# Kernel tuning notes

Hardware: AMD Instinct MI355X
Metric: run time of the kernel (lower is better)

The kernel has to match this reference:

```python
import jax, jax.numpy as jnp
import numpy as np

N, T, H, D, E, P, R = 50000, 16, 512, 256, 200000, 100000, 3
LN_EPS = 1e-5
BN_EPS = 1e-5


def setup_inputs() -> dict:
    key = jax.random.key(0)
    ks = jax.random.split(key, 32)
    ri = lambda k, shape, hi: jax.random.randint(k, shape, 0, hi)
    rn = lambda k, shape, scale=0.05: (jax.random.normal(k, shape, dtype=jnp.float32) * scale)
    return {
        "node_type_ids": ri(ks[0], (N,), T),
        "src0": ri(ks[1], (E,), N), "dst0": ri(ks[2], (E,), N),
        "src1": ri(ks[3], (E,), N), "dst1": ri(ks[4], (E,), N),
        "src2": ri(ks[5], (E,), N), "dst2": ri(ks[6], (E,), N),
        "pairs": ri(ks[7], (2, P), N),
        "degrees": ri(ks[8], (N,), 100),
        "node_emb": rn(ks[9], (N, H)),
        "type_emb": rn(ks[10], (T, H)),
        "w_loop_in": rn(ks[11], (H, H)),
        "w_rel_in": rn(ks[12], (R, H, H)),
        "w_loop_res": rn(ks[13], (H, H)),
        "w_rel_res": rn(ks[14], (R, H, H)),
        "ln_g": jnp.ones((H,), jnp.float32),
        "ln_b": jnp.zeros((H,), jnp.float32),
        "w_loop_out": rn(ks[15], (H, D)),
        "w_rel_out": rn(ks[16], (R, H, D)),
        "lp_w1": rn(ks[17], (3 * D, D)),
        "lp_b1": jnp.zeros((D,), jnp.float32),
        "bn_g": jnp.ones((D,), jnp.float32),
        "bn_b": jnp.zeros((D,), jnp.float32),
        "bn_mean": jnp.zeros((D,), jnp.float32),
        "bn_var": jnp.ones((D,), jnp.float32),
        "lp_w2": rn(ks[18], (D, 1)),
        "lp_b2": jnp.zeros((1,), jnp.float32),
        "alpha": jnp.float32(0.1),
        "beta": jnp.float32(0.1),
    }


def _rgcn(x, loop_w, rel_w, srcs, dsts):
    # out = x @ W_loop + sum_r (A_r @ x) @ W_r ; A_r unweighted COO -> segment_sum
    out = x @ loop_w
    for r in range(R):
        msg = jax.ops.segment_sum(x[srcs[r]], dsts[r], num_segments=x.shape[0])
        out = out + msg @ rel_w[r]
    return out


def _layernorm(h, g, b):
    mu = h.mean(-1, keepdims=True)
    var = h.var(-1, keepdims=True)
    return (h - mu) * jax.lax.rsqrt(var + LN_EPS) * g + b


def reference(node_type_ids, src0, dst0, src1, dst1, src2, dst2, pairs, degrees,
              node_emb, type_emb, w_loop_in, w_rel_in, w_loop_res, w_rel_res,
              ln_g, ln_b, w_loop_out, w_rel_out, lp_w1, lp_b1, bn_g, bn_b,
              bn_mean, bn_var, lp_w2, lp_b2, alpha, beta):
    srcs = (src0, src1, src2)
    dsts = (dst0, dst1, dst2)
    # encode
    x = node_emb + type_emb[node_type_ids]          # [N, H]
    x = jax.nn.relu(_rgcn(x, w_loop_in, w_rel_in, srcs, dsts))
    h = _rgcn(x, w_loop_res, w_rel_res, srcs, dsts)
    h = jax.nn.relu(_layernorm(h, ln_g, ln_b))      # dropout p=0 -> identity
    x = x + h
    z = _rgcn(x, w_loop_out, w_rel_out, srcs, dsts)  # [N, D]
    # score
    src_z = z[pairs[0]]                              # [P, D]
    dst_z = z[pairs[1]]
    src_deg = jnp.clip(degrees[pairs[0]], 1).astype(jnp.float32)
    dst_deg = jnp.clip(degrees[pairs[1]], 1).astype(jnp.float32)
    feats = jnp.concatenate([src_z, dst_z, src_z * dst_z], axis=-1)  # [P, 3D]
    h1 = jax.nn.relu(feats @ lp_w1 + lp_b1)
    # BatchNorm1d in eval mode: running stats
    h1 = (h1 - bn_mean) * jax.lax.rsqrt(bn_var + BN_EPS) * bn_g + bn_b
    mlp_score = (h1 @ lp_w2 + lp_b2).squeeze(-1)     # [P]
    base = mlp_score - jax.nn.relu(alpha) * jnp.log(src_deg) - jax.nn.relu(beta) * jnp.log(dst_deg)
    return base / (jnp.sqrt(src_deg) * jnp.sqrt(dst_deg) + 1e-8)
```

## Files before the change

### kernel.cpp

```cpp
#include <hip/hip_runtime.h>

typedef __attribute__((ext_vector_type(8))) _Float16 half8;
typedef __attribute__((ext_vector_type(4))) _Float16 half4;
typedef __attribute__((ext_vector_type(4))) float f32x4;

static __device__ __forceinline__ void gload16(const void* g, void* l) {
  __builtin_amdgcn_global_load_lds((const __attribute__((address_space(1))) void*)g,
                                   (__attribute__((address_space(3))) void*)l, 16, 0, 0);
}

__global__ void k_encode(const float* __restrict__ emb, const float* __restrict__ temb,
                         const int* __restrict__ tids, _Float16* __restrict__ x, int n) {
  int i = blockIdx.x * 256 + threadIdx.x;
  if (i >= n * 64) return;
  int node = i >> 6, c = (i & 63) << 3;
  const float* e = emb + (size_t)node * 512 + c;
  const float* t = temb + (size_t)tids[node] * 512 + c;
  float4 a0 = *(const float4*)e, a1 = *(const float4*)(e + 4);
  float4 b0 = *(const float4*)t, b1 = *(const float4*)(t + 4);
  half8 o;
  o[0] = (_Float16)(a0.x + b0.x); o[1] = (_Float16)(a0.y + b0.y);
  o[2] = (_Float16)(a0.z + b0.z); o[3] = (_Float16)(a0.w + b0.w);
  o[4] = (_Float16)(a1.x + b1.x); o[5] = (_Float16)(a1.y + b1.y);
  o[6] = (_Float16)(a1.z + b1.z); o[7] = (_Float16)(a1.w + b1.w);
  *(half8*)(x + (size_t)node * 512 + c) = o;
}

__global__ void k_hist(const int* __restrict__ d0, const int* __restrict__ d1,
                       const int* __restrict__ d2, int* __restrict__ counts, int E) {
  int e = blockIdx.x * 256 + threadIdx.x;
  if (e >= E) return;
  int r = blockIdx.y;
  const int* d = (r == 0) ? d0 : ((r == 1) ? d1 : d2);
  atomicAdd(&counts[d[e] + 1], 1);
}

__global__ void k_scan(const int* __restrict__ counts, int* __restrict__ rowp,
                       int* __restrict__ cursor, int n) {
  __shared__ int wsum[16];
  int lane = threadIdx.x & 63, w = threadIdx.x >> 6;
  int off = 0;
  for (int base = 0; base < n; base += 1024) {
    int i = base + threadIdx.x;
    int v = (i < n) ? counts[i] : 0;
    int sc = v;
    #pragma unroll
    for (int d = 1; d < 64; d <<= 1) {
      int t = __shfl_up(sc, (unsigned)d);
      if (lane >= d) sc += t;
    }
    if (lane == 63) wsum[w] = sc;
    __syncthreads();
    int wo = 0, tot = 0;
    #pragma unroll
    for (int ww = 0; ww < 16; ++ww) {
      int s = wsum[ww];
      if (ww < w) wo += s;
      tot += s;
    }
    if (i < n) { int val = sc + wo + off; rowp[i] = val; cursor[i] = val; }
    off += tot;
    __syncthreads();
  }
}

__global__ void k_fill(const int* __restrict__ s0, const int* __restrict__ s1, const int* __restrict__ s2,
                       const int* __restrict__ d0, const int* __restrict__ d1, const int* __restrict__ d2,
                       int* __restrict__ cursor, int* __restrict__ colrel, int E) {
  int e = blockIdx.x * 256 + threadIdx.x;
  if (e >= E) return;
  int r = blockIdx.y;
  const int* dp = (r == 0) ? d0 : ((r == 1) ? d1 : d2);
  const int* sp = (r == 0) ? s0 : ((r == 1) ? s1 : s2);
  int pos = atomicAdd(&cursor[dp[e]], 1);
  if (pos >= 0 && pos < 3 * E) colrel[pos] = sp[e] | (r << 24);
}

__global__ void k_aggregate(const _Float16* __restrict__ x, _Float16* __restrict__ agg,
                            const int* __restrict__ rowp, const int* __restrict__ colrel,
                            int N) {
  int wid = (blockIdx.x * 256 + threadIdx.x) >> 6;
  int lane = threadIdx.x & 63;
  if (wid >= N) return;
  int beg = rowp[wid], end = rowp[wid + 1];
  int co = lane * 8;
  float a0[8] = {0,0,0,0,0,0,0,0}, a1[8] = {0,0,0,0,0,0,0,0}, a2[8] = {0,0,0,0,0,0,0,0};
  int e = beg;
  for (; e + 4 <= end; e += 4) {
    int c0 = colrel[e], c1 = colrel[e + 1], c2 = colrel[e + 2], c3 = colrel[e + 3];
    half8 v0 = *(const half8*)(x + (size_t)(c0 & 0xFFFFFF) * 512 + co);
    half8 v1 = *(const half8*)(x + (size_t)(c1 & 0xFFFFFF) * 512 + co);
    half8 v2 = *(const half8*)(x + (size_t)(c2 & 0xFFFFFF) * 512 + co);
    half8 v3 = *(const half8*)(x + (size_t)(c3 & 0xFFFFFF) * 512 + co);
    {
      int r = c0 >> 24;
      if (r == 0) { for (int j = 0; j < 8; ++j) a0[j] += (float)v0[j]; }
      else if (r == 1) { for (int j = 0; j < 8; ++j) a1[j] += (float)v0[j]; }
      else { for (int j = 0; j < 8; ++j) a2[j] += (float)v0[j]; }
    }
    {
      int r = c1 >> 24;
      if (r == 0) { for (int j = 0; j < 8; ++j) a0[j] += (float)v1[j]; }
      else if (r == 1) { for (int j = 0; j < 8; ++j) a1[j] += (float)v1[j]; }
      else { for (int j = 0; j < 8; ++j) a2[j] += (float)v1[j]; }
    }
    {
      int r = c2 >> 24;
      if (r == 0) { for (int j = 0; j < 8; ++j) a0[j] += (float)v2[j]; }
      else if (r == 1) { for (int j = 0; j < 8; ++j) a1[j] += (float)v2[j]; }
      else { for (int j = 0; j < 8; ++j) a2[j] += (float)v2[j]; }
    }
    {
      int r = c3 >> 24;
      if (r == 0) { for (int j = 0; j < 8; ++j) a0[j] += (float)v3[j]; }
      else if (r == 1) { for (int j = 0; j < 8; ++j) a1[j] += (float)v3[j]; }
      else { for (int j = 0; j < 8; ++j) a2[j] += (float)v3[j]; }
    }
  }
  for (; e < end; ++e) {
    int c0 = colrel[e];
    half8 v0 = *(const half8*)(x + (size_t)(c0 & 0xFFFFFF) * 512 + co);
    int r = c0 >> 24;
    if (r == 0) { for (int j = 0; j < 8; ++j) a0[j] += (float)v0[j]; }
    else if (r == 1) { for (int j = 0; j < 8; ++j) a1[j] += (float)v0[j]; }
    else { for (int j = 0; j < 8; ++j) a2[j] += (float)v0[j]; }
  }
  half8 o0, o1, o2;
  #pragma unroll
  for (int j = 0; j < 8; ++j) {
    o0[j] = (_Float16)a0[j]; o1[j] = (_Float16)a1[j]; o2[j] = (_Float16)a2[j];
  }
  size_t ob = (size_t)wid * 1536;
  *(half8*)(agg + ob + co) = o0;
  *(half8*)(agg + ob + 512 + co) = o1;
  *(half8*)(agg + ob + 1024 + co) = o2;
}

__global__ void k_transpose_all(const float* __restrict__ wli, const float* __restrict__ wri,
                                const float* __restrict__ wlr, const float* __restrict__ wrr,
                                const float* __restrict__ wlo, const float* __restrict__ wro,
                                const float* __restrict__ lpw1,
                                _Float16* __restrict__ Bti, _Float16* __restrict__ Btr,
                                _Float16* __restrict__ Bto, _Float16* __restrict__ Btl) {
  __shared__ float tile[64][65];
  int zi = blockIdx.z;
  const float* Bl; const float* Br; _Float16* Bt; int No, K;
  if (zi == 0)      { Bl = wli;  Br = wri;            Bt = Bti; No = 512; K = 2048; }
  else if (zi == 1) { Bl = wlr;  Br = wrr;            Bt = Btr; No = 512; K = 2048; }
  else if (zi == 2) { Bl = wlo;  Br = wro;            Bt = Bto; No = 256; K = 2048; }
  else              { Bl = lpw1; Br = lpw1 + 512*256; Bt = Btl; No = 256; K = 768;  }
  int k0 = blockIdx.x * 64, n0 = blockIdx.y * 64;
  if (k0 >= K || n0 >= No) return;
  int nl = threadIdx.x & 63, kb = threadIdx.x >> 6;
  #pragma unroll
  for (int i = 0; i < 16; ++i) {
    int kl = kb + i * 4;
    int krow = k0 + kl;
    float v = (krow < 512) ? Bl[(size_t)krow * No + n0 + nl]
                           : Br[(size_t)(krow - 512) * No + n0 + nl];
    tile[kl][nl] = v;
  }
  __syncthreads();
  int kl = threadIdx.x & 63, nb = threadIdx.x >> 6;
  #pragma unroll
  for (int i = 0; i < 16; ++i) {
    int n2 = nb + i * 4;
    Bt[(size_t)(n0 + n2) * K + k0 + kl] = (_Float16)tile[kl][n2];
  }
}

__global__ __launch_bounds__(512) void k_gemm_rgcn(
    const _Float16* __restrict__ Ain, const _Float16* __restrict__ Aagg,
    const _Float16* __restrict__ Bt, _Float16* __restrict__ C,
    int M, int Ncols, int K, int relu, int S, int T) {
  __shared__ __align__(16) _Float16 As[256 * 64];
  __shared__ __align__(16) _Float16 Bs[128 * 64];
  int lin = blockIdx.x;
  int grp = lin / (8 * T);
  int rmd = lin - grp * 8 * T;
  int c = rmd >> 3, x = rmd & 7;
  int s = grp * 8 + x;
  if (s >= S) return;
  int bm0 = s * 256, bn0 = c * 128;

  int tid = threadIdx.x;
  int lane = tid & 63, wv = tid >> 6;
  int wm = wv & 3, wn = wv >> 2;
  int l16 = lane & 15, quad = lane >> 4;

  int rl8 = lane >> 3;
  int gs = (lane & 7) ^ rl8;

  int rA[4];
  const _Float16* pa[4];
  const _Float16* pb[2];
  _Float16* ldA[4];
  _Float16* ldB[2];
  #pragma unroll
  for (int q = 0; q < 4; ++q) {
    int chunk = wv * 4 + q;
    int rl = chunk * 8 + rl8;
    int ra = bm0 + rl; if (ra >= M) ra = M - 1;
    rA[q] = ra;
    pa[q] = Ain + (size_t)ra * 512 + gs * 8;
    ldA[q] = &As[chunk * 8 * 64];
  }
  #pragma unroll
  for (int q = 0; q < 2; ++q) {
    int chunk = wv * 2 + q;
    int rl = chunk * 8 + rl8;
    pb[q] = Bt + (size_t)(bn0 + rl) * K + gs * 8;
    ldB[q] = &Bs[chunk * 8 * 64];
  }

  f32x4 acc[4][4];
  #pragma unroll
  for (int i = 0; i < 4; ++i)
    #pragma unroll
    for (int j = 0; j < 4; ++j) acc[i][j] = (f32x4){0.f, 0.f, 0.f, 0.f};

  for (int k0 = 0; k0 < K; k0 += 64) {
    if (k0 == 512) {
      #pragma unroll
      for (int q = 0; q < 4; ++q) pa[q] = Aagg + (size_t)rA[q] * 1536 + gs * 8;
    }
    __syncthreads();
    #pragma unroll
    for (int q = 0; q < 4; ++q) gload16(pa[q], ldA[q]);
    #pragma unroll
    for (int q = 0; q < 2; ++q) gload16(pb[q], ldB[q]);
    __syncthreads();
    #pragma unroll
    for (int sb = 0; sb < 2; ++sb) {
      half8 af[4], bf[4];
      int slot = ((sb * 4 + quad) ^ (l16 & 7)) * 8;
      #pragma unroll
      for (int i = 0; i < 4; ++i)
        af[i] = *(const half8*)&As[(wm * 64 + i * 16 + l16) * 64 + slot];
      #pragma unroll
      for (int j = 0; j < 4; ++j)
        bf[j] = *(const half8*)&Bs[(wn * 64 + j * 16 + l16) * 64 + slot];
      #pragma unroll
      for (int i = 0; i < 4; ++i)
        #pragma unroll
        for (int j = 0; j < 4; ++j)
          acc[i][j] = __builtin_amdgcn_mfma_f32_16x16x32_f16(af[i], bf[j], acc[i][j], 0, 0, 0);
    }
    #pragma unroll
    for (int q = 0; q < 4; ++q) pa[q] += 64;
    #pragma unroll
    for (int q = 0; q < 2; ++q) pb[q] += 64;
  }

  #pragma unroll
  for (int i = 0; i < 4; ++i)
    #pragma unroll
    for (int j = 0; j < 4; ++j)
      #pragma unroll
      for (int rg = 0; rg < 4; ++rg) {
        int row = bm0 + wm * 64 + i * 16 + quad * 4 + rg;
        int col = bn0 + wn * 64 + j * 16 + l16;
        if (row < M) {
          float v = acc[i][j][rg];
          if (relu) v = fmaxf(v, 0.f);
          C[(size_t)row * Ncols + col] = (_Float16)v;
        }
      }
}

#define LSTR 40

__global__ __launch_bounds__(256) void k_gemm_link(
    const _Float16* __restrict__ z, const int* __restrict__ pairs,
    const _Float16* __restrict__ Bt,
    const float* __restrict__ b1, const float* __restrict__ bng, const float* __restrict__ bnb,
    const float* __restrict__ bnm, const float* __restrict__ bnv,
    _Float16* __restrict__ h1, int P, int K) {
  __shared__ __align__(16) _Float16 As[128 * LSTR];
  __shared__ __align__(16) _Float16 Bs[128 * LSTR];
  int tid = threadIdx.x;
  int bn0 = blockIdx.x * 128, bm0 = blockIdx.y * 128;
  int lane = tid & 63, wv = tid >> 6;
  int wm = wv & 1, wn = wv >> 1;
  int l16 = lane & 15, quad = lane >> 4;
  int srow = tid >> 1, scs = (tid & 1) * 16;
  int p = bm0 + srow; if (p >= P) p = P - 1;
  int sp = pairs[p], dp = pairs[P + p];
  const _Float16* zs = z + (size_t)sp * 256;
  const _Float16* zd = z + (size_t)dp * 256;
  int bgn = bn0 + srow;

  f32x4 acc[4][4];
  #pragma unroll
  for (int i = 0; i < 4; ++i)
    #pragma unroll
    for (int j = 0; j < 4; ++j) acc[i][j] = (f32x4){0.f, 0.f, 0.f, 0.f};

  for (int k0 = 0; k0 < K; k0 += 32) {
    __syncthreads();
    int seg = k0 >> 8;
    int kk = (k0 & 255) + scs;
    __attribute__((aligned(16))) _Float16 tmp[16];
    if (seg == 0) {
      *(uint4*)tmp = *(const uint4*)(zs + kk);
      *(uint4*)(tmp + 8) = *(const uint4*)(zs + kk + 8);
    } else if (seg == 1) {
      *(uint4*)tmp = *(const uint4*)(zd + kk);
      *(uint4*)(tmp + 8) = *(const uint4*)(zd + kk + 8);
    } else {
      half8 u0 = *(const half8*)(zs + kk), u1 = *(const half8*)(zs + kk + 8);
      half8 v0 = *(const half8*)(zd + kk), v1 = *(const half8*)(zd + kk + 8);
      #pragma unroll
      for (int j = 0; j < 8; ++j) {
        tmp[j] = (_Float16)((float)u0[j] * (float)v0[j]);
        tmp[j + 8] = (_Float16)((float)u1[j] * (float)v1[j]);
      }
    }
    *(uint4*)&As[srow * LSTR + scs] = *(const uint4*)tmp;
    *(uint4*)&As[srow * LSTR + scs + 8] = *(const uint4*)(tmp + 8);
    {
      const _Float16* src = Bt + (size_t)bgn * K + k0 + scs;
      *(uint4*)&Bs[srow * LSTR + scs] = *(const uint4*)src;
      *(uint4*)&Bs[srow * LSTR + scs + 8] = *(const uint4*)(src + 8);
    }
    __syncthreads();
    half8 af[4], bf[4];
    #pragma unroll
    for (int i = 0; i < 4; ++i)
      af[i] = *(const half8*)&As[(wm * 64 + i * 16 + l16) * LSTR + quad * 8];
    #pragma unroll
    for (int j = 0; j < 4; ++j)
      bf[j] = *(const half8*)&Bs[(wn * 64 + j * 16 + l16) * LSTR + quad * 8];
    #pragma unroll
    for (int i = 0; i < 4; ++i)
      #pragma unroll
      for (int j = 0; j < 4; ++j)
        acc[i][j] = __builtin_amdgcn_mfma_f32_16x16x32_f16(af[i], bf[j], acc[i][j], 0, 0, 0);
  }

  #pragma unroll
  for (int i = 0; i < 4; ++i)
    #pragma unroll
    for (int j = 0; j < 4; ++j) {
      int col = bn0 + wn * 64 + j * 16 + l16;
      float bb1 = b1[col], m = bnm[col], rs = rsqrtf(bnv[col] + 1e-5f);
      float gg = bng[col], bb = bnb[col];
      #pragma unroll
      for (int rg = 0; rg < 4; ++rg) {
        int row = bm0 + wm * 64 + i * 16 + quad * 4 + rg;
        if (row < P) {
          float v = fmaxf(acc[i][j][rg] + bb1, 0.f);
          v = (v - m) * rs * gg + bb;
          h1[(size_t)row * 256 + col] = (_Float16)v;
        }
      }
    }
}

__global__ void k_ln_res(const _Float16* __restrict__ h, const _Float16* __restrict__ x1,
                         const float* __restrict__ g, const float* __restrict__ b,
                         _Float16* __restrict__ out, int N) {
  int wid = (blockIdx.x * 256 + threadIdx.x) >> 6;
  int lane = threadIdx.x & 63;
  if (wid >= N) return;
  int c = lane * 8;
  half8 hv = *(const half8*)(h + (size_t)wid * 512 + c);
  float hf[8];
  float s = 0.f, sq = 0.f;
  #pragma unroll
  for (int j = 0; j < 8; ++j) {
    hf[j] = (float)hv[j];
    s += hf[j];
    sq += hf[j] * hf[j];
  }
  #pragma unroll
  for (int off = 32; off; off >>= 1) {
    s += __shfl_down(s, (unsigned)off);
    sq += __shfl_down(sq, (unsigned)off);
  }
  s = __shfl(s, 0); sq = __shfl(sq, 0);
  float mu = s * (1.f / 512.f);
  float var = sq * (1.f / 512.f) - mu * mu;
  float rs = rsqrtf(var + 1e-5f);
  float4 g0 = *(const float4*)(g + c), g1 = *(const float4*)(g + c + 4);
  float4 b0 = *(const float4*)(b + c), b1 = *(const float4*)(b + c + 4);
  float gf[8] = {g0.x, g0.y, g0.z, g0.w, g1.x, g1.y, g1.z, g1.w};
  float bf[8] = {b0.x, b0.y, b0.z, b0.w, b1.x, b1.y, b1.z, b1.w};
  half8 xv = *(const half8*)(x1 + (size_t)wid * 512 + c);
  half8 o;
  #pragma unroll
  for (int j = 0; j < 8; ++j) {
    float xw = (float)xv[j];
    o[j] = (_Float16)(xw + fmaxf((hf[j] - mu) * rs * gf[j] + bf[j], 0.f));
  }
  *(half8*)(out + (size_t)wid * 512 + c) = o;
}

__global__ void k_score(const _Float16* __restrict__ h1, const float* __restrict__ w2,
                        const float* __restrict__ b2, const int* __restrict__ pairs,
                        const int* __restrict__ degrees, const float* __restrict__ alpha,
                        const float* __restrict__ beta, float* __restrict__ out, int P) {
  int wid = (blockIdx.x * 256 + threadIdx.x) >> 6;
  int lane = threadIdx.x & 63;
  if (wid >= P) return;
  int c = lane * 4;
  half4 hv = *(const half4*)(h1 + (size_t)wid * 256 + c);
  float4 wv = *(const float4*)(w2 + c);
  float s = (float)hv[0] * wv.x + (float)hv[1] * wv.y + (float)hv[2] * wv.z + (float)hv[3] * wv.w;
  #pragma unroll
  for (int off = 32; off; off >>= 1) s += __shfl_down(s, (unsigned)off);
  if (lane == 0) {
    int sp = pairs[wid], dp = pairs[P + wid];
    float sd = (float)max(degrees[sp], 1);
    float dd = (float)max(degrees[dp], 1);
    float base = s + b2[0] - fmaxf(alpha[0], 0.f) * logf(sd) - fmaxf(beta[0], 0.f) * logf(dd);
    out[wid] = base / (sqrtf(sd) * sqrtf(dd) + 1e-8f);
  }
}

extern "C" void kernel_launch(void* const* d_in, const int* in_sizes, int n_in,
                              void* d_out, int out_size, void* d_ws, size_t ws_size,
                              hipStream_t stream) {
  const int N = 50000, E = 200000, P = 100000;
  const int Np1 = N + 1;
  const int* node_type = (const int*)d_in[0];
  const int* src0 = (const int*)d_in[1]; const int* dst0 = (const int*)d_in[2];
  const int* src1 = (const int*)d_in[3]; const int* dst1 = (const int*)d_in[4];
  const int* src2 = (const int*)d_in[5]; const int* dst2 = (const int*)d_in[6];
  const int* pairs = (const int*)d_in[7];
  const int* degrees = (const int*)d_in[8];
  const float* node_emb = (const float*)d_in[9];
  const float* type_emb = (const float*)d_in[10];
  const float* w_loop_in = (const float*)d_in[11];
  const float* w_rel_in = (const float*)d_in[12];
  const float* w_loop_res = (const float*)d_in[13];
  const float* w_rel_res = (const float*)d_in[14];
  const float* ln_g = (const float*)d_in[15];
  const float* ln_b = (const float*)d_in[16];
  const float* w_loop_out = (const float*)d_in[17];
  const float* w_rel_out = (const float*)d_in[18];
  const float* lp_w1 = (const float*)d_in[19];
  const float* lp_b1 = (const float*)d_in[20];
  const float* bn_g = (const float*)d_in[21];
  const float* bn_b = (const float*)d_in[22];
  const float* bn_mean = (const float*)d_in[23];
  const float* bn_var = (const float*)d_in[24];
  const float* lp_w2 = (const float*)d_in[25];
  const float* lp_b2 = (const float*)d_in[26];
  const float* alpha = (const float*)d_in[27];
  const float* beta = (const float*)d_in[28];
  float* out = (float*)d_out;

  char* ws = (char*)d_ws;
  size_t off = 0;
  auto alloc = [&](size_t bytes) {
    void* p = ws + off;
    off = (off + bytes + 255) & ~(size_t)255;
    return p;
  };
  _Float16* xb0 = (_Float16*)alloc((size_t)N * 512 * 2);
  _Float16* xb1 = (_Float16*)alloc((size_t)N * 512 * 2);
  _Float16* agg = (_Float16*)alloc((size_t)N * 1536 * 2);
  _Float16* Bti = (_Float16*)alloc((size_t)512 * 2048 * 2);
  _Float16* Btr = (_Float16*)alloc((size_t)512 * 2048 * 2);
  _Float16* Bto = (_Float16*)alloc((size_t)256 * 2048 * 2);
  _Float16* Btl = (_Float16*)alloc((size_t)256 * 768 * 2);
  int* counts = (int*)alloc((size_t)Np1 * 4);
  int* rowp = (int*)alloc((size_t)Np1 * 4);
  int* cursor = (int*)alloc((size_t)Np1 * 4);
  int* colrel = (int*)alloc((size_t)3 * E * 4);
  if (off > ws_size) return;

  _Float16* z = xb1;
  _Float16* h1 = agg;

  k_transpose_all<<<dim3(32, 8, 4), 256, 0, stream>>>(
      w_loop_in, w_rel_in, w_loop_res, w_rel_res, w_loop_out, w_rel_out, lp_w1,
      Bti, Btr, Bto, Btl);

  hipMemsetAsync(counts, 0, (size_t)Np1 * 4, stream);
  dim3 gE((E + 255) / 256, 3);
  k_hist<<<gE, 256, 0, stream>>>(dst0, dst1, dst2, counts, E);
  k_scan<<<1, 1024, 0, stream>>>(counts, rowp, cursor, Np1);
  k_fill<<<gE, 256, 0, stream>>>(src0, src1, src2, dst0, dst1, dst2, cursor, colrel, E);

  k_encode<<<(N * 64 + 255) / 256, 256, 0, stream>>>(node_emb, type_emb, node_type, xb0, N);

  int aggBlocks = (N + 3) / 4;
  const int S = (N + 255) / 256;
  int blocks4 = ((S + 7) / 8) * 8 * 4;
  int blocks2 = ((S + 7) / 8) * 8 * 2;

  k_aggregate<<<aggBlocks, 256, 0, stream>>>(xb0, agg, rowp, colrel, N);
  k_gemm_rgcn<<<blocks4, 512, 0, stream>>>(xb0, agg, Bti, xb1, N, 512, 2048, 1, S, 4);

  k_aggregate<<<aggBlocks, 256, 0, stream>>>(xb1, agg, rowp, colrel, N);
  k_gemm_rgcn<<<blocks4, 512, 0, stream>>>(xb1, agg, Btr, xb0, N, 512, 2048, 0, S, 4);

  k_ln_res<<<(N + 3) / 4, 256, 0, stream>>>(xb0, xb1, ln_g, ln_b, xb0, N);

  k_aggregate<<<aggBlocks, 256, 0, stream>>>(xb0, agg, rowp, colrel, N);
  k_gemm_rgcn<<<blocks2, 512, 0, stream>>>(xb0, agg, Bto, z, N, 256, 2048, 0, S, 2);

  dim3 gl(2, (P + 127) / 128);
  k_gemm_link<<<gl, 256, 0, stream>>>(z, pairs, Btl, lp_b1, bn_g, bn_b, bn_mean, bn_var, h1, P, 768);

  k_score<<<(P + 3) / 4, 256, 0, stream>>>(h1, lp_w2, lp_b2, pairs, degrees, alpha, beta, out, P);
}
```

Measured before the change: 1.074 ms.

## Load link-predictor MFMA fragments directly from global memory, drop LDS staging

The link-prediction GEMM no longer stages A (gathered z rows and their product) and B tiles through shared memory with two barriers per k-step. Each lane now loads its MFMA operand fragments straight from global memory via per-row pointers, and the block grows to 512 threads covering 256 pair rows. This removes LDS traffic and synchronisation, but global loads become less coalesced (16-byte pieces per lane across scattered rows). B tiles are also fetched redundantly by every wave instead of being shared.

```diff
diff --git a/kernel.cpp b/kernel.cpp
--- a/kernel.cpp
+++ b/kernel.cpp
@@ -268,27 +268,31 @@
       }
 }
 
-#define LSTR 40
-
-__global__ __launch_bounds__(256) void k_gemm_link(
+__global__ __launch_bounds__(512) void k_gemm_link(
     const _Float16* __restrict__ z, const int* __restrict__ pairs,
     const _Float16* __restrict__ Bt,
     const float* __restrict__ b1, const float* __restrict__ bng, const float* __restrict__ bnb,
     const float* __restrict__ bnm, const float* __restrict__ bnv,
     _Float16* __restrict__ h1, int P, int K) {
-  __shared__ __align__(16) _Float16 As[128 * LSTR];
-  __shared__ __align__(16) _Float16 Bs[128 * LSTR];
   int tid = threadIdx.x;
-  int bn0 = blockIdx.x * 128, bm0 = blockIdx.y * 128;
+  int bn0 = blockIdx.x * 128, bm0 = blockIdx.y * 256;
   int lane = tid & 63, wv = tid >> 6;
-  int wm = wv & 1, wn = wv >> 1;
+  int wm = wv & 3, wn = wv >> 2;
   int l16 = lane & 15, quad = lane >> 4;
-  int srow = tid >> 1, scs = (tid & 1) * 16;
-  int p = bm0 + srow; if (p >= P) p = P - 1;
-  int sp = pairs[p], dp = pairs[P + p];
-  const _Float16* zs = z + (size_t)sp * 256;
-  const _Float16* zd = z + (size_t)dp * 256;
-  int bgn = bn0 + srow;
+
+  const _Float16* zsp[4];
+  const _Float16* zdp[4];
+  #pragma unroll
+  for (int i = 0; i < 4; ++i) {
+    int row = bm0 + wm * 64 + i * 16 + l16;
+    if (row >= P) row = P - 1;
+    zsp[i] = z + (size_t)pairs[row] * 256;
+    zdp[i] = z + (size_t)pairs[P + row] * 256;
+  }
+  const _Float16* bp[4];
+  #pragma unroll
+  for (int j = 0; j < 4; ++j)
+    bp[j] = Bt + (size_t)(bn0 + wn * 64 + j * 16 + l16) * K + quad * 8;
 
   f32x4 acc[4][4];
   #pragma unroll
@@ -297,40 +301,26 @@
     for (int j = 0; j < 4; ++j) acc[i][j] = (f32x4){0.f, 0.f, 0.f, 0.f};
 
   for (int k0 = 0; k0 < K; k0 += 32) {
-    __syncthreads();
     int seg = k0 >> 8;
-    int kk = (k0 & 255) + scs;
-    __attribute__((aligned(16))) _Float16 tmp[16];
+    int kk = (k0 & 255) + quad * 8;
+    half8 af[4], bf[4];
     if (seg == 0) {
-      *(uint4*)tmp = *(const uint4*)(zs + kk);
-      *(uint4*)(tmp + 8) = *(const uint4*)(zs + kk + 8);
+      #pragma unroll
+      for (int i = 0; i < 4; ++i) af[i] = *(const half8*)(zsp[i] + kk);
     } else if (seg == 1) {
-      *(uint4*)tmp = *(const uint4*)(zd + kk);
-      *(uint4*)(tmp + 8) = *(const uint4*)(zd + kk + 8);
+      #pragma unroll
+      for (int i = 0; i < 4; ++i) af[i] = *(const half8*)(zdp[i] + kk);
     } else {
-      half8 u0 = *(const half8*)(zs + kk), u1 = *(const half8*)(zs + kk + 8);
-      half8 v0 = *(const half8*)(zd + kk), v1 = *(const half8*)(zd + kk + 8);
-      #pragma unroll
-      for (int j = 0; j < 8; ++j) {
-        tmp[j] = (_Float16)((float)u0[j] * (float)v0[j]);
-        tmp[j + 8] = (_Float16)((float)u1[j] * (float)v1[j]);
+      #pragma unroll
+      for (int i = 0; i < 4; ++i) {
+        half8 u = *(const half8*)(zsp[i] + kk);
+        half8 v = *(const half8*)(zdp[i] + kk);
+        #pragma unroll
+        for (int j = 0; j < 8; ++j) af[i][j] = (_Float16)((float)u[j] * (float)v[j]);
       }
     }
-    *(uint4*)&As[srow * LSTR + scs] = *(const uint4*)tmp;
-    *(uint4*)&As[srow * LSTR + scs + 8] = *(const uint4*)(tmp + 8);
-    {
-      const _Float16* src = Bt + (size_t)bgn * K + k0 + scs;
-      *(uint4*)&Bs[srow * LSTR + scs] = *(const uint4*)src;
-      *(uint4*)&Bs[srow * LSTR + scs + 8] = *(const uint4*)(src + 8);
-    }
-    __syncthreads();
-    half8 af[4], bf[4];
-    #pragma unroll
-    for (int i = 0; i < 4; ++i)
-      af[i] = *(const half8*)&As[(wm * 64 + i * 16 + l16) * LSTR + quad * 8];
-    #pragma unroll
-    for (int j = 0; j < 4; ++j)
-      bf[j] = *(const half8*)&Bs[(wn * 64 + j * 16 + l16) * LSTR + quad * 8];
+    #pragma unroll
+    for (int j = 0; j < 4; ++j) bf[j] = *(const half8*)(bp[j] + k0);
     #pragma unroll
     for (int i = 0; i < 4; ++i)
       #pragma unroll
@@ -339,12 +329,12 @@
   }
 
   #pragma unroll
-  for (int i = 0; i < 4; ++i)
-    #pragma unroll
-    for (int j = 0; j < 4; ++j) {
-      int col = bn0 + wn * 64 + j * 16 + l16;
-      float bb1 = b1[col], m = bnm[col], rs = rsqrtf(bnv[col] + 1e-5f);
-      float gg = bng[col], bb = bnb[col];
+  for (int j = 0; j < 4; ++j) {
+    int col = bn0 + wn * 64 + j * 16 + l16;
+    float bb1 = b1[col], m = bnm[col], rs = rsqrtf(bnv[col] + 1e-5f);
+    float gg = bng[col], bb = bnb[col];
+    #pragma unroll
+    for (int i = 0; i < 4; ++i)
       #pragma unroll
       for (int rg = 0; rg < 4; ++rg) {
         int row = bm0 + wm * 64 + i * 16 + quad * 4 + rg;
@@ -354,7 +344,7 @@
           h1[(size_t)row * 256 + col] = (_Float16)v;
         }
       }
-    }
+  }
 }
 
 __global__ void k_ln_res(const _Float16* __restrict__ h, const _Float16* __restrict__ x1,
@@ -502,8 +492,8 @@
   k_aggregate<<<aggBlocks, 256, 0, stream>>>(xb0, agg, rowp, colrel, N);
   k_gemm_rgcn<<<blocks2, 512, 0, stream>>>(xb0, agg, Bto, z, N, 256, 2048, 0, S, 2);
 
-  dim3 gl(2, (P + 127) / 128);
-  k_gemm_link<<<gl, 256, 0, stream>>>(z, pairs, Btl, lp_b1, bn_g, bn_b, bn_mean, bn_var, h1, P, 768);
+  dim3 gl(2, (P + 255) / 256);
+  k_gemm_link<<<gl, 512, 0, stream>>>(z, pairs, Btl, lp_b1, bn_g, bn_b, bn_mean, bn_var, h1, P, 768);
 
   k_score<<<(P + 3) / 4, 256, 0, stream>>>(h1, lp_w2, lp_b2, pairs, degrees, alpha, beta, out, P);
 }
```

After: 1.204 ms. +12.1%, slower.
